# Performance work log

Measured on AMD Instinct MI355X. Metric: run time of the kernel, lower is better.

Reference implementation:

```python
import jax, jax.numpy as jnp
import numpy as np


def setup_inputs() -> dict:
    key = jax.random.key(0)
    k1, k2, k3, k4, k5 = jax.random.split(key, 5)
    B, TQ, TK, DQ, DV, U = 4, 512, 512, 512, 512, 256
    query = jax.random.normal(k1, (B, TQ, DQ), dtype=jnp.float32)
    value = jax.random.normal(k2, (B, TK, DV), dtype=jnp.float32)
    W1 = jax.random.normal(k3, (DQ, U), dtype=jnp.float32) * (1.0 / np.sqrt(DQ))
    W2 = jax.random.normal(k4, (DV, U), dtype=jnp.float32) * (1.0 / np.sqrt(DV))
    scale = jax.random.normal(k5, (U,), dtype=jnp.float32)
    return {"query": query, "value": value, "W1": W1, "W2": W2, "scale": scale}


def reference(query, value, W1, W2, scale):
    # Dense projections (no bias)
    q = jnp.einsum('bqd,du->bqu', query, W1)   # [B, Tq, U]
    k = jnp.einsum('bkd,du->bku', value, W2)   # [B, Tk, U]
    # Keras AdditiveAttention (use_scale=True):
    # scores[b,q,k] = sum_u scale[u] * tanh(q[b,q,u] + k[b,k,u])
    t = jnp.tanh(q[:, :, None, :] + k[:, None, :, :])  # [B, Tq, Tk, U]
    scores = jnp.einsum('bqku,u->bqk', t, scale)        # [B, Tq, Tk]
    attention_weights = jax.nn.softmax(scores, axis=-1)
    return attention_weights
```

## Files before the change

### kernel.cpp

```cpp
#include <hip/hip_runtime.h>

#define BB 4
#define TQ 512
#define TK 512
#define DQ 512
#define UU 256
#define CSC 2.8853900817779268f
#define L2E 1.4426950408889634f
#define RQ 2

typedef unsigned short u16;
typedef unsigned int u32;
typedef short bf16x8 __attribute__((ext_vector_type(8)));
typedef float f32x4 __attribute__((ext_vector_type(4)));

__device__ __forceinline__ float fexp2(float x) { return __builtin_amdgcn_exp2f(x); }
__device__ __forceinline__ float frcp(float x)  { return __builtin_amdgcn_rcpf(x); }
__device__ __forceinline__ u32 pkhi(u32 a, u32 b) { return (b & 0xffff0000u) | (a >> 16); }

__global__ __launch_bounds__(256) void proj2(
    const float* __restrict__ Aq, const float* __restrict__ Av,
    const float* __restrict__ W1, const float* __restrict__ W2,
    float* __restrict__ Eq, float* __restrict__ Ek)
{
    __shared__ __align__(16) char raw[28672];
    float* fin = (float*)raw;

    const int z = blockIdx.z;
    const float* A = z ? Av : Aq;
    const float* W = z ? W2 : W1;

    const int t = threadIdx.x;
    const int m0 = blockIdx.x * 32, n0 = blockIdx.y * 64;
    const int wave = t >> 6, ln = t & 15, qd = (t & 63) >> 4;
    const int arow = t >> 3, ak4 = (t & 7) * 4;
    const int wk = t >> 4, wn4 = (t & 15) * 4;

    f32x4 acc[2] = {};

    float4 a4  = *(const float4*)&A[(size_t)(m0 + arow) * DQ + ak4];
    float4 w40 = *(const float4*)&W[(size_t)wk * UU + n0 + wn4];
    float4 w41 = *(const float4*)&W[(size_t)(16 + wk) * UU + n0 + wn4];

    for (int i = 0; i < DQ / 32; i++) {
        char* buf = raw + (i & 1) * 14336;
        u16*   Ah_s = (u16*)buf;
        u16*   Al_s = (u16*)(buf + 2560);
        float* Ws_s = (float*)(buf + 5120);
        {
            const float f[4] = {a4.x, a4.y, a4.z, a4.w};
            u32 x[4], lx[4];
            #pragma unroll
            for (int e = 0; e < 4; e++) {
                x[e]  = __float_as_uint(f[e]);
                lx[e] = __float_as_uint(f[e] - __uint_as_float(x[e] & 0xffff0000u));
            }
            uint2 hw, lw;
            hw.x = pkhi(x[0], x[1]);  hw.y = pkhi(x[2], x[3]);
            lw.x = pkhi(lx[0], lx[1]); lw.y = pkhi(lx[2], lx[3]);
            *(uint2*)&Ah_s[arow * 40 + ak4] = hw;
            *(uint2*)&Al_s[arow * 40 + ak4] = lw;
        }
        *(float4*)&Ws_s[wk * 72 + wn4] = w40;
        *(float4*)&Ws_s[(wk + 16) * 72 + wn4] = w41;

        if (i + 1 < DQ / 32) {
            const int k0 = (i + 1) * 32;
            a4  = *(const float4*)&A[(size_t)(m0 + arow) * DQ + k0 + ak4];
            w40 = *(const float4*)&W[(size_t)(k0 + wk) * UU + n0 + wn4];
            w41 = *(const float4*)&W[(size_t)(k0 + 16 + wk) * UU + n0 + wn4];
        }
        __syncthreads();

        bf16x8 ah[2], al[2], bh, bl;
        #pragma unroll
        for (int ii = 0; ii < 2; ii++) {
            const int ar = (ii * 16 + ln) * 40 + qd * 8;
            ah[ii] = *(const bf16x8*)&Ah_s[ar];
            al[ii] = *(const bf16x8*)&Al_s[ar];
        }
        {
            const int cl = wave * 16 + ln;
            float wf[8];
            #pragma unroll
            for (int e = 0; e < 8; e++) wf[e] = Ws_s[(qd * 8 + e) * 72 + cl];
            u32 y[8], ly[8];
            #pragma unroll
            for (int e = 0; e < 8; e++) {
                y[e]  = __float_as_uint(wf[e]);
                ly[e] = __float_as_uint(wf[e] - __uint_as_float(y[e] & 0xffff0000u));
            }
            union { uint4 u; bf16x8 v; } h, l;
            h.u.x = pkhi(y[0], y[1]);  h.u.y = pkhi(y[2], y[3]);
            h.u.z = pkhi(y[4], y[5]);  h.u.w = pkhi(y[6], y[7]);
            l.u.x = pkhi(ly[0], ly[1]); l.u.y = pkhi(ly[2], ly[3]);
            l.u.z = pkhi(ly[4], ly[5]); l.u.w = pkhi(ly[6], ly[7]);
            bh = h.v; bl = l.v;
        }
        #pragma unroll
        for (int ii = 0; ii < 2; ii++) {
            acc[ii] = __builtin_amdgcn_mfma_f32_16x16x32_bf16(ah[ii], bh, acc[ii], 0, 0, 0);
            acc[ii] = __builtin_amdgcn_mfma_f32_16x16x32_bf16(ah[ii], bl, acc[ii], 0, 0, 0);
            acc[ii] = __builtin_amdgcn_mfma_f32_16x16x32_bf16(al[ii], bh, acc[ii], 0, 0, 0);
        }
    }

    const int ncol = n0 + wave * 16 + ln;
    if (z == 0) {
        #pragma unroll
        for (int ii = 0; ii < 2; ii++) {
            #pragma unroll
            for (int r = 0; r < 4; r++) {
                const int m = m0 + ii * 16 + qd * 4 + r;
                Eq[(size_t)m * UU + ncol] = fexp2(CSC * acc[ii][r]);
            }
        }
    } else {
        __syncthreads();
        #pragma unroll
        for (int ii = 0; ii < 2; ii++) {
            #pragma unroll
            for (int r = 0; r < 4; r++) {
                const int ml = ii * 16 + qd * 4 + r;
                const int nl = wave * 16 + ln;
                fin[ml * 68 + nl] = fexp2(CSC * acc[ii][r]);
            }
        }
        __syncthreads();
        const int b = m0 >> 9, j0 = m0 & 511;
        #pragma unroll
        for (int p = 0; p < 2; p++) {
            const int idx = p * 256 + t;
            const int jl = idx & 31, u4 = idx >> 5;
            const float4 v = *(const float4*)&fin[jl * 68 + u4 * 4];
            ((float4*)Ek)[(size_t)(b * (UU / 4) + (n0 >> 2) + u4) * TK + j0 + jl] = v;
        }
    }
}

__global__ __launch_bounds__(512) void attn_softmax(
    const float* __restrict__ Eq,
    const float* __restrict__ Ek,
    const float* __restrict__ scale,
    float* __restrict__ out)
{
    __shared__ float redbuf[RQ][8];
    const int t  = threadIdx.x;
    const int b  = blockIdx.x >> 8;
    const int q0 = (blockIdx.x & 255) * RQ;
    const float*  qrow = Eq + (size_t)(b * TQ + q0) * UU;
    const float4* kb4  = (const float4*)Ek + (size_t)b * (UU / 4) * TK + t;

    float acc[RQ] = {};
    float4 kbuf[2];
    kbuf[0] = kb4[0];
    kbuf[1] = kb4[TK];

    #pragma unroll 2
    for (int g = 0; g < UU / 4; g++) {
        const float4 kv = kbuf[g & 1];
        if (g + 2 < UU / 4) kbuf[g & 1] = kb4[(size_t)(g + 2) * TK];
        const float4 sc4 = *(const float4*)&scale[4 * g];
        const float* sf = (const float*)&sc4;
        const float* kf = (const float*)&kv;
        #pragma unroll
        for (int r = 0; r < RQ; r++) {
            const float4 q4 = *(const float4*)&qrow[(size_t)r * UU + 4 * g];
            const float* qf = (const float*)&q4;
            #pragma unroll
            for (int p = 0; p < 4; p += 2) {
                const float d0 = fmaf(qf[p],     kf[p],     1.0f);
                const float d1 = fmaf(qf[p + 1], kf[p + 1], 1.0f);
                const float num = fmaf(sf[p], d1, sf[p + 1] * d0);
                acc[r] = fmaf(num, frcp(d0 * d1), acc[r]);
            }
        }
    }
    #pragma unroll
    for (int r = 0; r < RQ; r++) acc[r] *= -2.0f;

    const int wave = t >> 6, lane = t & 63;
    float m[RQ], p[RQ];

    #pragma unroll
    for (int r = 0; r < RQ; r++) {
        float v = acc[r];
        #pragma unroll
        for (int o = 32; o > 0; o >>= 1) v = fmaxf(v, __shfl_xor(v, o));
        if (lane == 0) redbuf[r][wave] = v;
    }
    __syncthreads();
    #pragma unroll
    for (int r = 0; r < RQ; r++) {
        float v = redbuf[r][0];
        #pragma unroll
        for (int w = 1; w < 8; w++) v = fmaxf(v, redbuf[r][w]);
        m[r] = v;
    }
    __syncthreads();

    #pragma unroll
    for (int r = 0; r < RQ; r++) {
        p[r] = fexp2(L2E * (acc[r] - m[r]));
        float v = p[r];
        #pragma unroll
        for (int o = 32; o > 0; o >>= 1) v += __shfl_xor(v, o);
        if (lane == 0) redbuf[r][wave] = v;
    }
    __syncthreads();
    #pragma unroll
    for (int r = 0; r < RQ; r++) {
        float v = 0.0f;
        #pragma unroll
        for (int w = 0; w < 8; w++) v += redbuf[r][w];
        const float rinv = frcp(v);
        out[(size_t)(b * TQ + q0 + r) * TK + t] = p[r] * rinv;
    }
}

extern "C" void kernel_launch(void* const* d_in, const int* in_sizes, int n_in,
                              void* d_out, int out_size, void* d_ws, size_t ws_size,
                              hipStream_t stream) {
    const float* query = (const float*)d_in[0];
    const float* value = (const float*)d_in[1];
    const float* W1    = (const float*)d_in[2];
    const float* W2    = (const float*)d_in[3];
    const float* scale = (const float*)d_in[4];
    float* out = (float*)d_out;

    float* Eq = (float*)d_ws;
    float* Ek = Eq + (size_t)BB * TQ * UU;
    (void)ws_size;

    proj2<<<dim3(64, 4, 2), 256, 0, stream>>>(query, value, W1, W2, Eq, Ek);
    attn_softmax<<<dim3(BB * TQ / RQ), 512, 0, stream>>>(Eq, Ek, scale, out);
}
```

Baseline: 109.9 us.

## Pre-split weights into transposed bf16 hi/lo and deepen Ek prefetch

Adds a small kernel that converts W1/W2 once per call into transposed bf16 high/low halves, so the projection kernel loads ready-made MFMA B operands straight from global memory. This removes the weight staging through shared memory and the per-block split work, and shrinks LDS use. The attention kernel now prefetches four Ek vectors ahead instead of two, to hide more load latency. The cost is an extra kernel launch and the extra workspace traffic for the split weights.

```diff
diff --git a/kernel.cpp b/kernel.cpp
--- a/kernel.cpp
+++ b/kernel.cpp
@@ -18,35 +18,67 @@
 __device__ __forceinline__ float frcp(float x)  { return __builtin_amdgcn_rcpf(x); }
 __device__ __forceinline__ u32 pkhi(u32 a, u32 b) { return (b & 0xffff0000u) | (a >> 16); }
 
-__global__ __launch_bounds__(256) void proj2(
+__global__ __launch_bounds__(256) void wsplit(
+    const float* __restrict__ W1, const float* __restrict__ W2,
+    u16* __restrict__ W1h, u16* __restrict__ W1l,
+    u16* __restrict__ W2h, u16* __restrict__ W2l)
+{
+    __shared__ float tile[32][33];
+    const int blk = blockIdx.x, t = threadIdx.x;
+    const float* W = (blk >> 7) ? W2 : W1;
+    u16* oh = (blk >> 7) ? W2h : W1h;
+    u16* ol = (blk >> 7) ? W2l : W1l;
+    const int tl = blk & 127;
+    const int k0 = (tl >> 3) * 32, n0 = (tl & 7) * 32;
+    const int kl = t >> 5, nl = t & 31;
+    #pragma unroll
+    for (int r = 0; r < 4; r++)
+        tile[kl + 8 * r][nl] = W[(size_t)(k0 + kl + 8 * r) * UU + n0 + nl];
+    __syncthreads();
+    const int nr = t >> 5, kc = t & 31;
+    #pragma unroll
+    for (int r = 0; r < 4; r++) {
+        const float v = tile[kc][nr + 8 * r];
+        const u32 x = __float_as_uint(v);
+        const u16 h = (u16)(x >> 16);
+        const u16 l = (u16)(__float_as_uint(v - __uint_as_float(x & 0xffff0000u)) >> 16);
+        oh[(size_t)(n0 + nr + 8 * r) * DQ + k0 + kc] = h;
+        ol[(size_t)(n0 + nr + 8 * r) * DQ + k0 + kc] = l;
+    }
+}
+
+__global__ __launch_bounds__(256) void proj3(
     const float* __restrict__ Aq, const float* __restrict__ Av,
-    const float* __restrict__ W1, const float* __restrict__ W2,
+    const u16* __restrict__ W1h, const u16* __restrict__ W1l,
+    const u16* __restrict__ W2h, const u16* __restrict__ W2l,
     float* __restrict__ Eq, float* __restrict__ Ek)
 {
-    __shared__ __align__(16) char raw[28672];
+    __shared__ __align__(16) char raw[10240];
     float* fin = (float*)raw;
 
     const int z = blockIdx.z;
     const float* A = z ? Av : Aq;
-    const float* W = z ? W2 : W1;
+    const u16* Wh = z ? W2h : W1h;
+    const u16* Wl = z ? W2l : W1l;
 
     const int t = threadIdx.x;
     const int m0 = blockIdx.x * 32, n0 = blockIdx.y * 64;
     const int wave = t >> 6, ln = t & 15, qd = (t & 63) >> 4;
     const int arow = t >> 3, ak4 = (t & 7) * 4;
-    const int wk = t >> 4, wn4 = (t & 15) * 4;
+    const int ncol = n0 + wave * 16 + ln;
+    const u16* whp = Wh + (size_t)ncol * DQ + qd * 8;
+    const u16* wlp = Wl + (size_t)ncol * DQ + qd * 8;
 
     f32x4 acc[2] = {};
 
-    float4 a4  = *(const float4*)&A[(size_t)(m0 + arow) * DQ + ak4];
-    float4 w40 = *(const float4*)&W[(size_t)wk * UU + n0 + wn4];
-    float4 w41 = *(const float4*)&W[(size_t)(16 + wk) * UU + n0 + wn4];
+    float4 a4 = *(const float4*)&A[(size_t)(m0 + arow) * DQ + ak4];
+    bf16x8 whc = *(const bf16x8*)&whp[0];
+    bf16x8 wlc = *(const bf16x8*)&wlp[0];
 
     for (int i = 0; i < DQ / 32; i++) {
-        char* buf = raw + (i & 1) * 14336;
-        u16*   Ah_s = (u16*)buf;
-        u16*   Al_s = (u16*)(buf + 2560);
-        float* Ws_s = (float*)(buf + 5120);
+        char* buf = raw + (i & 1) * 5120;
+        u16* Ah_s = (u16*)buf;
+        u16* Al_s = (u16*)(buf + 2560);
         {
             const float f[4] = {a4.x, a4.y, a4.z, a4.w};
             u32 x[4], lx[4];
@@ -61,51 +93,32 @@
             *(uint2*)&Ah_s[arow * 40 + ak4] = hw;
             *(uint2*)&Al_s[arow * 40 + ak4] = lw;
         }
-        *(float4*)&Ws_s[wk * 72 + wn4] = w40;
-        *(float4*)&Ws_s[(wk + 16) * 72 + wn4] = w41;
-
+        if (i + 1 < DQ / 32)
+            a4 = *(const float4*)&A[(size_t)(m0 + arow) * DQ + (i + 1) * 32 + ak4];
+        __syncthreads();
+
+        bf16x8 whn, wln;
         if (i + 1 < DQ / 32) {
-            const int k0 = (i + 1) * 32;
-            a4  = *(const float4*)&A[(size_t)(m0 + arow) * DQ + k0 + ak4];
-            w40 = *(const float4*)&W[(size_t)(k0 + wk) * UU + n0 + wn4];
-            w41 = *(const float4*)&W[(size_t)(k0 + 16 + wk) * UU + n0 + wn4];
-        }
-        __syncthreads();
-
-        bf16x8 ah[2], al[2], bh, bl;
+            whn = *(const bf16x8*)&whp[(i + 1) * 32];
+            wln = *(const bf16x8*)&wlp[(i + 1) * 32];
+        }
+
+        bf16x8 ah[2], al[2];
         #pragma unroll
         for (int ii = 0; ii < 2; ii++) {
             const int ar = (ii * 16 + ln) * 40 + qd * 8;
             ah[ii] = *(const bf16x8*)&Ah_s[ar];
             al[ii] = *(const bf16x8*)&Al_s[ar];
         }
-        {
-            const int cl = wave * 16 + ln;
-            float wf[8];
-            #pragma unroll
-            for (int e = 0; e < 8; e++) wf[e] = Ws_s[(qd * 8 + e) * 72 + cl];
-            u32 y[8], ly[8];
-            #pragma unroll
-            for (int e = 0; e < 8; e++) {
-                y[e]  = __float_as_uint(wf[e]);
-                ly[e] = __float_as_uint(wf[e] - __uint_as_float(y[e] & 0xffff0000u));
-            }
-            union { uint4 u; bf16x8 v; } h, l;
-            h.u.x = pkhi(y[0], y[1]);  h.u.y = pkhi(y[2], y[3]);
-            h.u.z = pkhi(y[4], y[5]);  h.u.w = pkhi(y[6], y[7]);
-            l.u.x = pkhi(ly[0], ly[1]); l.u.y = pkhi(ly[2], ly[3]);
-            l.u.z = pkhi(ly[4], ly[5]); l.u.w = pkhi(ly[6], ly[7]);
-            bh = h.v; bl = l.v;
-        }
-        #pragma unroll
-        for (int ii = 0; ii < 2; ii++) {
-            acc[ii] = __builtin_amdgcn_mfma_f32_16x16x32_bf16(ah[ii], bh, acc[ii], 0, 0, 0);
-            acc[ii] = __builtin_amdgcn_mfma_f32_16x16x32_bf16(ah[ii], bl, acc[ii], 0, 0, 0);
-            acc[ii] = __builtin_amdgcn_mfma_f32_16x16x32_bf16(al[ii], bh, acc[ii], 0, 0, 0);
-        }
-    }
-
-    const int ncol = n0 + wave * 16 + ln;
+        #pragma unroll
+        for (int ii = 0; ii < 2; ii++) {
+            acc[ii] = __builtin_amdgcn_mfma_f32_16x16x32_bf16(ah[ii], whc, acc[ii], 0, 0, 0);
+            acc[ii] = __builtin_amdgcn_mfma_f32_16x16x32_bf16(ah[ii], wlc, acc[ii], 0, 0, 0);
+            acc[ii] = __builtin_amdgcn_mfma_f32_16x16x32_bf16(al[ii], whc, acc[ii], 0, 0, 0);
+        }
+        whc = whn; wlc = wln;
+    }
+
     if (z == 0) {
         #pragma unroll
         for (int ii = 0; ii < 2; ii++) {
@@ -152,14 +165,8 @@
     const float4* kb4  = (const float4*)Ek + (size_t)b * (UU / 4) * TK + t;
 
     float acc[RQ] = {};
-    float4 kbuf[2];
-    kbuf[0] = kb4[0];
-    kbuf[1] = kb4[TK];
-
-    #pragma unroll 2
-    for (int g = 0; g < UU / 4; g++) {
-        const float4 kv = kbuf[g & 1];
-        if (g + 2 < UU / 4) kbuf[g & 1] = kb4[(size_t)(g + 2) * TK];
+
+    auto body = [&](const float4& kv, int g) {
         const float4 sc4 = *(const float4*)&scale[4 * g];
         const float* sf = (const float*)&sc4;
         const float* kf = (const float*)&kv;
@@ -175,6 +182,22 @@
                 acc[r] = fmaf(num, frcp(d0 * d1), acc[r]);
             }
         }
+    };
+
+    float4 c0 = kb4[0];
+    float4 c1 = kb4[(size_t)TK];
+    float4 c2 = kb4[(size_t)2 * TK];
+    float4 c3 = kb4[(size_t)3 * TK];
+    for (int g = 0; g < UU / 4; g += 4) {
+        float4 n0v, n1v, n2v, n3v;
+        if (g + 4 < UU / 4) {
+            n0v = kb4[(size_t)(g + 4) * TK];
+            n1v = kb4[(size_t)(g + 5) * TK];
+            n2v = kb4[(size_t)(g + 6) * TK];
+            n3v = kb4[(size_t)(g + 7) * TK];
+        }
+        body(c0, g); body(c1, g + 1); body(c2, g + 2); body(c3, g + 3);
+        c0 = n0v; c1 = n1v; c2 = n2v; c3 = n3v;
     }
     #pragma unroll
     for (int r = 0; r < RQ; r++) acc[r] *= -2.0f;
@@ -230,8 +253,14 @@
 
     float* Eq = (float*)d_ws;
     float* Ek = Eq + (size_t)BB * TQ * UU;
+    char* wbase = (char*)d_ws + 4 * 1048576;
+    u16* W1h = (u16*)(wbase);
+    u16* W1l = (u16*)(wbase + 262144);
+    u16* W2h = (u16*)(wbase + 524288);
+    u16* W2l = (u16*)(wbase + 786432);
     (void)ws_size;
 
-    proj2<<<dim3(64, 4, 2), 256, 0, stream>>>(query, value, W1, W2, Eq, Ek);
+    wsplit<<<256, 256, 0, stream>>>(W1, W2, W1h, W1l, W2h, W2l);
+    proj3<<<dim3(64, 4, 2), 256, 0, stream>>>(query, value, W1h, W1l, W2h, W2l, Eq, Ek);
     attn_softmax<<<dim3(BB * TQ / RQ), 512, 0, stream>>>(Eq, Ek, scale, out);
 }
```

Measured after the change: 107.9 us. No clear change (-1.8%).
